# Kernel optimization log

Hardware: AMD Instinct MI355X
Metric: run time of the kernel (lower is better)

The kernel has to match this reference:

```python
import jax, jax.numpy as jnp
import numpy as np

EPS = 1e-8


def setup_inputs() -> dict:
    key = jax.random.key(0)
    k1, k2 = jax.random.split(key)
    N, F, K, C = 16384, 64, 32, 100
    membership = jax.random.uniform(k1, (N, F, K), dtype=jnp.float32)
    teacher_probs = jax.random.uniform(k2, (N, C), dtype=jnp.float32)
    return {"membership": membership, "teacher_probs": teacher_probs}


def reference(membership, teacher_probs):
    # membership: [N, F, K]  soft bin assignments per feature
    # teacher_probs: [N, C]  teacher class distribution per sample
    N, F, K = membership.shape
    bin_mass = membership.sum(axis=0) + EPS  # [F, K]
    # Contraction form of (membership[:, :, :, None] * teacher_probs[:, None, None, :]).sum(0)
    # avoids the N*F*K*C intermediate.
    centroids = jnp.einsum('nfk,nc->fkc', membership, teacher_probs) / bin_mass[:, :, None]  # [F, K, C]
    # Intra-bin: minimize entropy of each bin's class distribution, mass-weighted.
    intra_entropy = -jnp.sum(centroids * jnp.log(centroids + EPS), axis=2)  # [F, K]
    loss_intra = jnp.sum(intra_entropy * bin_mass) / N
    # Inter-bin: maximize entropy of the mixture of adjacent bins
    # (loss_inter is negative entropy summed, added with +0.5 weight).
    mixture = 0.5 * (centroids[:, :-1, :] + centroids[:, 1:, :])  # [F, K-1, C]
    loss_inter = jnp.sum(mixture * jnp.log(mixture + EPS))
    return loss_intra + 0.5 * loss_inter
```

## Files before the change

### kernel.cpp

```cpp
#include <hip/hip_runtime.h>
#include <hip/hip_bf16.h>

#define NS   16384
#define FKD  2048
#define CD   100
#define CP   112
#define NKC  32
#define PHASES 16
#define EPSF 1e-8f
#define SFK  (FKD * CP)
#define NGRP (NS / 8)
#define WBUF 1024

typedef float f32x4 __attribute__((ext_vector_type(4)));
typedef short bf16x8 __attribute__((ext_vector_type(8)));
typedef unsigned uint4v __attribute__((ext_vector_type(4)));

__device__ inline unsigned short f2bf(float f) {
    unsigned int u = __float_as_uint(f);
    u += 0x7FFFu + ((u >> 16) & 1u);
    return (unsigned short)(u >> 16);
}

__device__ __forceinline__ void gload16(const float* g, const float* l) {
    __builtin_amdgcn_global_load_lds(
        (const __attribute__((address_space(1))) void*)g,
        (__attribute__((address_space(3))) void*)l, 16, 0, 0);
}

__global__ __launch_bounds__(256) void ebl_prep(
    const float* __restrict__ tp, unsigned short* __restrict__ Bp,
    unsigned* __restrict__ cnt)
{
    const int idx = blockIdx.x * 256 + threadIdx.x;
    if (idx == 0) *cnt = 0;
    if (idx >= NGRP * CP) return;
    const int g = idx / CP, c = idx - g * CP;
    unsigned short v[8];
    if (c < CD) {
        const float* p = tp + (size_t)g * 8 * CD + c;
        #pragma unroll
        for (int j = 0; j < 8; ++j) v[j] = f2bf(p[(size_t)j * CD]);
    } else {
        const unsigned short fill = (c == CD) ? 0x3F80 : 0;
        #pragma unroll
        for (int j = 0; j < 8; ++j) v[j] = fill;
    }
    *reinterpret_cast<uint4*>(Bp + (size_t)idx * 8) = *reinterpret_cast<const uint4*>(v);
}

__global__ __launch_bounds__(128) void ebl_gemm(
    const float* __restrict__ mem, const unsigned short* __restrict__ Bp,
    unsigned short* __restrict__ spart)
{
    __shared__ float At[4 * 2 * WBUF];

    const int t  = threadIdx.x;
    const int w  = t >> 6;
    const int l  = t & 63;
    const int lg = l >> 4, lr = l & 15;
    const int m0 = blockIdx.x * 64;
    const int kc = blockIdx.y;
    const int n0 = kc * (PHASES * 32);
    const int gb = n0 >> 3;

    const float* gbase = mem + (size_t)(n0 + (l >> 3)) * FKD + (m0 + w * 32 + (l & 7) * 4);

    f32x4 acc[2][7];
    #pragma unroll
    for (int i = 0; i < 2; ++i)
        #pragma unroll
        for (int nt = 0; nt < 7; ++nt) acc[i][nt] = (f32x4){0.f, 0.f, 0.f, 0.f};

    bf16x8 b0[7], b1[7];

#define SB() __builtin_amdgcn_sched_barrier(0)
#define BUFO(p) ((((p) & 3) * 2 + w) * WBUF)
#define STAGE(p) { \
    const float* gs = gbase + (size_t)(p) * 32 * FKD; \
    const int bo_ = BUFO(p); \
    _Pragma("unroll") \
    for (int q = 0; q < 4; ++q) \
        gload16(gs + (size_t)q * 8 * FKD, At + bo_ + q * 256); \
    SB(); }
#define LOADB(dst, p) { \
    const unsigned short* bq = Bp + ((size_t)(gb + (p) * 4 + lg) * CP + lr) * 8; \
    _Pragma("unroll") \
    for (int nt = 0; nt < 7; ++nt) dst[nt] = *reinterpret_cast<const bf16x8*>(bq + nt * 128); \
    SB(); }
#define WAITV(n) { asm volatile("s_waitcnt vmcnt(" #n ")" ::: "memory"); SB(); }
#define COMPUTE(p, bB) { \
    const int bo_ = BUFO(p); \
    bf16x8 af[2]; \
    _Pragma("unroll") \
    for (int i = 0; i < 2; ++i) { \
        uint4v u; \
        _Pragma("unroll") \
        for (int jj = 0; jj < 4; ++jj) { \
            float f0 = At[bo_ + ((2 * lg + (jj >> 1)) * 4 + 2 * (jj & 1))     * 32 + i * 16 + lr]; \
            float f1 = At[bo_ + ((2 * lg + (jj >> 1)) * 4 + 2 * (jj & 1) + 1) * 32 + i * 16 + lr]; \
            unsigned uu; \
            asm("v_cvt_pk_bf16_f32 %0, %1, %2" : "=v"(uu) : "v"(f0), "v"(f1)); \
            u[jj] = uu; \
        } \
        af[i] = __builtin_bit_cast(bf16x8, u); \
    } \
    SB(); \
    _Pragma("unroll") \
    for (int i = 0; i < 2; ++i) \
        _Pragma("unroll") \
        for (int nt = 0; nt < 7; ++nt) \
            acc[i][nt] = __builtin_amdgcn_mfma_f32_16x16x32_bf16(af[i], bB[nt], acc[i][nt], 0, 0, 0); }

    STAGE(0)
    STAGE(1)
    LOADB(b0, 0)
    STAGE(2)

    for (int ph = 0; ph < PHASES - 3; ++ph) {
        LOADB(b1, ph + 1)
        STAGE(ph + 3)
        WAITV(15)
        COMPUTE(ph, b0)
        #pragma unroll
        for (int nt = 0; nt < 7; ++nt) b0[nt] = b1[nt];
    }
    LOADB(b1, PHASES - 2)
    WAITV(11)
    COMPUTE(PHASES - 3, b0)
    #pragma unroll
    for (int nt = 0; nt < 7; ++nt) b0[nt] = b1[nt];
    LOADB(b1, PHASES - 1)
    WAITV(7)
    COMPUTE(PHASES - 2, b0)
    WAITV(0)
    COMPUTE(PHASES - 1, b1)

#undef SB
#undef BUFO
#undef STAGE
#undef LOADB
#undef WAITV
#undef COMPUTE

    unsigned short* sp = spart + (size_t)kc * SFK;
    #pragma unroll
    for (int i = 0; i < 2; ++i) {
        #pragma unroll
        for (int nt = 0; nt < 7; ++nt) {
            const int c = nt * 16 + lr;
            #pragma unroll
            for (int r = 0; r < 4; ++r) {
                const int mm = m0 + w * 32 + i * 16 + lg * 4 + r;
                sp[(size_t)mm * CP + c] = f2bf(acc[i][nt][r]);
            }
        }
    }
}

__global__ __launch_bounds__(256) void ebl_tail(
    const unsigned short* __restrict__ spart, float* __restrict__ fpart,
    unsigned* __restrict__ cnt, float* __restrict__ out)
{
    __shared__ float Ss[32 * CP];
    __shared__ float massL[32];
    __shared__ float red[4];
    __shared__ int lastFlag;
    const int t = threadIdx.x;
    const int f = blockIdx.x;
    const size_t base = (size_t)f * 32 * CP;

    for (int v = t; v < 32 * CP / 8; v += 256) {
        float s[8];
        #pragma unroll
        for (int j = 0; j < 8; ++j) s[j] = 0.f;
        for (int p = 0; p < NKC; ++p) {
            uint4 raw = *reinterpret_cast<const uint4*>(spart + (size_t)p * SFK + base + (size_t)v * 8);
            const unsigned short* u = reinterpret_cast<const unsigned short*>(&raw);
            #pragma unroll
            for (int j = 0; j < 8; ++j) s[j] += __uint_as_float((unsigned)u[j] << 16);
        }
        #pragma unroll
        for (int j = 0; j < 8; ++j) Ss[v * 8 + j] = s[j];
    }
    __syncthreads();
    if (t < 32) massL[t] = Ss[t * CP + CD] + EPSF;
    __syncthreads();

    float a_int = 0.f, a_mix = 0.f;
    for (int idx = t; idx < 32 * CD; idx += 256) {
        const int k = idx / CD, c = idx - k * CD;
        const float cent = Ss[k * CP + c] / massL[k];
        a_int -= cent * logf(cent + EPSF) * massL[k];
    }
    for (int idx = t; idx < 31 * CD; idx += 256) {
        const int k = idx / CD, c = idx - k * CD;
        const float mix = 0.5f * (Ss[k * CP + c] / massL[k] + Ss[(k + 1) * CP + c] / massL[k + 1]);
        a_mix += mix * logf(mix + EPSF);
    }

    float part = a_int * (1.0f / (float)NS) + 0.5f * a_mix;
    #pragma unroll
    for (int off = 32; off > 0; off >>= 1) part += __shfl_down(part, off);
    if ((t & 63) == 0) red[t >> 6] = part;
    __syncthreads();

    if (t == 0) {
        fpart[f] = (red[0] + red[1]) + (red[2] + red[3]);
        __threadfence();
        const unsigned ticket =
            __hip_atomic_fetch_add(cnt, 1u, __ATOMIC_ACQ_REL, __HIP_MEMORY_SCOPE_AGENT);
        lastFlag = (ticket == 63);
    }
    __syncthreads();

    if (lastFlag && t < 64) {
        float v = __hip_atomic_load(&fpart[t], __ATOMIC_ACQUIRE, __HIP_MEMORY_SCOPE_AGENT);
        #pragma unroll
        for (int off = 32; off > 0; off >>= 1) v += __shfl_down(v, off);
        if (t == 0) out[0] = v;
    }
}

extern "C" void kernel_launch(void* const* d_in, const int* in_sizes, int n_in,
                              void* d_out, int out_size, void* d_ws, size_t ws_size,
                              hipStream_t stream)
{
    const float* mem = (const float*)d_in[0];
    const float* tp  = (const float*)d_in[1];
    float* out = (float*)d_out;

    const size_t bpBytes = (size_t)NGRP * CP * 8 * 2;

    unsigned short* Bp    = (unsigned short*)d_ws;
    unsigned short* spart = (unsigned short*)((char*)d_ws + bpBytes);
    float*          fpart = (float*)((char*)spart + (size_t)NKC * SFK * 2);
    unsigned*       cnt   = (unsigned*)(fpart + 64);

    ebl_prep<<<(NGRP * CP + 255) / 256, 256, 0, stream>>>(tp, Bp, cnt);
    dim3 grid(FKD / 64, NKC);
    ebl_gemm<<<grid, 128, 0, stream>>>(mem, Bp, spart);
    ebl_tail<<<64, 256, 0, stream>>>(spart, fpart, cnt, out);
}
```

Baseline: 52.61 us.

## Halve K-split count, triple-buffer LDS with padded chunks, unroll pipeline by two

Reduces the number of N-splits from 32 to 16 so each GEMM block runs 32 phases, which halves the bf16 partial-sum traffic written by the GEMM and read by the tail. LDS staging goes from four buffers to three rotating buffers. Each 8-row chunk is padded to 264 floats, which changes the LDS read pattern and is meant to avoid bank conflicts. The main loop is unrolled by two so the B fragments alternate between registers instead of being copied. One sched barrier inside COMPUTE is removed. The risks are fewer blocks in the grid, which lowers parallelism, and a shallower prefetch depth.

```diff
diff --git a/kernel.cpp b/kernel.cpp
--- a/kernel.cpp
+++ b/kernel.cpp
@@ -5,12 +5,13 @@
 #define FKD  2048
 #define CD   100
 #define CP   112
-#define NKC  32
-#define PHASES 16
+#define NKC  16
+#define PHASES 32
 #define EPSF 1e-8f
 #define SFK  (FKD * CP)
 #define NGRP (NS / 8)
-#define WBUF 1024
+#define CHUNK 264
+#define WBUF  (4 * CHUNK)
 
 typedef float f32x4 __attribute__((ext_vector_type(4)));
 typedef short bf16x8 __attribute__((ext_vector_type(8)));
@@ -53,7 +54,7 @@
     const float* __restrict__ mem, const unsigned short* __restrict__ Bp,
     unsigned short* __restrict__ spart)
 {
-    __shared__ float At[4 * 2 * WBUF];
+    __shared__ float At[3 * 2 * WBUF];
 
     const int t  = threadIdx.x;
     const int w  = t >> 6;
@@ -73,15 +74,14 @@
         for (int nt = 0; nt < 7; ++nt) acc[i][nt] = (f32x4){0.f, 0.f, 0.f, 0.f};
 
     bf16x8 b0[7], b1[7];
+    int o0 = (0 * 2 + w) * WBUF, o1 = (1 * 2 + w) * WBUF, o2 = (2 * 2 + w) * WBUF;
 
 #define SB() __builtin_amdgcn_sched_barrier(0)
-#define BUFO(p) ((((p) & 3) * 2 + w) * WBUF)
-#define STAGE(p) { \
+#define STAGE(bo, p) { \
     const float* gs = gbase + (size_t)(p) * 32 * FKD; \
-    const int bo_ = BUFO(p); \
     _Pragma("unroll") \
     for (int q = 0; q < 4; ++q) \
-        gload16(gs + (size_t)q * 8 * FKD, At + bo_ + q * 256); \
+        gload16(gs + (size_t)q * 8 * FKD, At + (bo) + q * CHUNK); \
     SB(); }
 #define LOADB(dst, p) { \
     const unsigned short* bq = Bp + ((size_t)(gb + (p) * 4 + lg) * CP + lr) * 8; \
@@ -89,55 +89,49 @@
     for (int nt = 0; nt < 7; ++nt) dst[nt] = *reinterpret_cast<const bf16x8*>(bq + nt * 128); \
     SB(); }
 #define WAITV(n) { asm volatile("s_waitcnt vmcnt(" #n ")" ::: "memory"); SB(); }
-#define COMPUTE(p, bB) { \
-    const int bo_ = BUFO(p); \
+#define COMPUTE(bo, bB) { \
     bf16x8 af[2]; \
     _Pragma("unroll") \
     for (int i = 0; i < 2; ++i) { \
         uint4v u; \
         _Pragma("unroll") \
         for (int jj = 0; jj < 4; ++jj) { \
-            float f0 = At[bo_ + ((2 * lg + (jj >> 1)) * 4 + 2 * (jj & 1))     * 32 + i * 16 + lr]; \
-            float f1 = At[bo_ + ((2 * lg + (jj >> 1)) * 4 + 2 * (jj & 1) + 1) * 32 + i * 16 + lr]; \
+            float f0 = At[(bo) + lg * CHUNK + (2 * jj)     * 32 + i * 16 + lr]; \
+            float f1 = At[(bo) + lg * CHUNK + (2 * jj + 1) * 32 + i * 16 + lr]; \
             unsigned uu; \
             asm("v_cvt_pk_bf16_f32 %0, %1, %2" : "=v"(uu) : "v"(f0), "v"(f1)); \
             u[jj] = uu; \
         } \
         af[i] = __builtin_bit_cast(bf16x8, u); \
     } \
-    SB(); \
     _Pragma("unroll") \
     for (int i = 0; i < 2; ++i) \
         _Pragma("unroll") \
         for (int nt = 0; nt < 7; ++nt) \
             acc[i][nt] = __builtin_amdgcn_mfma_f32_16x16x32_bf16(af[i], bB[nt], acc[i][nt], 0, 0, 0); }
 
-    STAGE(0)
-    STAGE(1)
+    STAGE(o0, 0)
     LOADB(b0, 0)
-    STAGE(2)
-
-    for (int ph = 0; ph < PHASES - 3; ++ph) {
+    STAGE(o1, 1)
+
+    for (int ph = 0; ph < PHASES - 2; ph += 2) {
         LOADB(b1, ph + 1)
-        STAGE(ph + 3)
+        STAGE(o2, ph + 2)
         WAITV(15)
-        COMPUTE(ph, b0)
-        #pragma unroll
-        for (int nt = 0; nt < 7; ++nt) b0[nt] = b1[nt];
-    }
-    LOADB(b1, PHASES - 2)
+        COMPUTE(o0, b0)
+        LOADB(b0, ph + 2)
+        STAGE(o0, ph + 3)
+        WAITV(15)
+        COMPUTE(o1, b1)
+        const int tmp = o2; o2 = o1; o1 = o0; o0 = tmp;
+    }
+    LOADB(b1, PHASES - 1)
     WAITV(11)
-    COMPUTE(PHASES - 3, b0)
-    #pragma unroll
-    for (int nt = 0; nt < 7; ++nt) b0[nt] = b1[nt];
-    LOADB(b1, PHASES - 1)
-    WAITV(7)
-    COMPUTE(PHASES - 2, b0)
+    COMPUTE(o0, b0)
     WAITV(0)
-    COMPUTE(PHASES - 1, b1)
+    COMPUTE(o1, b1)
 
 #undef SB
-#undef BUFO
 #undef STAGE
 #undef LOADB
 #undef WAITV
```

After: 53.21 us. No clear change (+1.2%).
